# Performance work log

Measured on AMD Instinct MI355X. Metric: run time of the kernel, lower is better.

## Reference

```python
import jax, jax.numpy as jnp
import numpy as np

N_MASTER = 100000
N_BOND = 200000
N_GLOB = 5000
E1 = 400000
E2 = 100000
D_IN = 64
D_OUT = 64
H = 4
SLOPE = 0.2  # leaky relu negative slope


def _mlp(x, W0, b0, W1, b1, W2):
    # LinearN with num_fc_layers=3: ELU, ELU, Identity (last layer no bias)
    h = jax.nn.elu(x @ W0 + b0)
    h = jax.nn.elu(h @ W1 + b1)
    return h @ W2  # (N, H*D_OUT)


def setup_inputs() -> dict:
    key = jax.random.key(0)
    ks = jax.random.split(key, 32)
    s = 0.1  # weight scale
    d = {
        "master_feats": jax.random.normal(ks[0], (N_MASTER, D_IN), jnp.float32),
        "bond_feats": jax.random.normal(ks[1], (N_BOND, D_IN), jnp.float32),
        "global_feats": jax.random.normal(ks[2], (N_GLOB, D_IN), jnp.float32),
        "atom_W0": jax.random.normal(ks[3], (D_IN, D_OUT), jnp.float32) * s,
        "atom_b0": jnp.zeros((D_OUT,), jnp.float32),
        "atom_W1": jax.random.normal(ks[4], (D_OUT, D_OUT), jnp.float32) * s,
        "atom_b1": jnp.zeros((D_OUT,), jnp.float32),
        "atom_W2": jax.random.normal(ks[5], (D_OUT, H * D_OUT), jnp.float32) * s,
        "bond_W0": jax.random.normal(ks[6], (D_IN, D_OUT), jnp.float32) * s,
        "bond_b0": jnp.zeros((D_OUT,), jnp.float32),
        "bond_W1": jax.random.normal(ks[7], (D_OUT, D_OUT), jnp.float32) * s,
        "bond_b1": jnp.zeros((D_OUT,), jnp.float32),
        "bond_W2": jax.random.normal(ks[8], (D_OUT, H * D_OUT), jnp.float32) * s,
        "glob_W0": jax.random.normal(ks[9], (D_IN, D_OUT), jnp.float32) * s,
        "glob_b0": jnp.zeros((D_OUT,), jnp.float32),
        "glob_W1": jax.random.normal(ks[10], (D_OUT, D_OUT), jnp.float32) * s,
        "glob_b1": jnp.zeros((D_OUT,), jnp.float32),
        "glob_W2": jax.random.normal(ks[11], (D_OUT, H * D_OUT), jnp.float32) * s,
        "attn_l": jax.random.normal(ks[12], (H, D_OUT), jnp.float32) * s,
        "attn_r": jax.random.normal(ks[13], (H, D_OUT), jnp.float32) * s,
        "e1_src": jax.random.randint(ks[14], (E1,), 0, N_BOND, jnp.int32),
        "e1_dst": jax.random.randint(ks[15], (E1,), 0, N_MASTER, jnp.int32),
        "e2_src": jax.random.randint(ks[16], (E2,), 0, N_GLOB, jnp.int32),
        "e2_dst": jax.random.randint(ks[17], (E2,), 0, N_MASTER, jnp.int32),
    }
    return d


def reference(master_feats, bond_feats, global_feats,
              atom_W0, atom_b0, atom_W1, atom_b1, atom_W2,
              bond_W0, bond_b0, bond_W1, bond_b1, bond_W2,
              glob_W0, glob_b0, glob_W1, glob_b1, glob_W2,
              attn_l, attn_r, e1_src, e1_dst, e2_src, e2_dst):
    # Per-node-type projections to (N, H, D_OUT)
    ft_m = _mlp(master_feats, atom_W0, atom_b0, atom_W1, atom_b1, atom_W2).reshape(N_MASTER, H, D_OUT)
    ft_b = _mlp(bond_feats, bond_W0, bond_b0, bond_W1, bond_b1, bond_W2).reshape(N_BOND, H, D_OUT)
    ft_g = _mlp(global_feats, glob_W0, glob_b0, glob_W1, glob_b1, glob_W2).reshape(N_GLOB, H, D_OUT)

    er = jnp.einsum('nhd,hd->nh', ft_m, attn_r)  # master (dst) scores
    el_b = jnp.einsum('nhd,hd->nh', ft_b, attn_l)
    el_g = jnp.einsum('nhd,hd->nh', ft_g, attn_l)

    # Per-edge logits: u_add_v then leaky relu
    e1 = jax.nn.leaky_relu(el_b[e1_src] + er[e1_dst], negative_slope=SLOPE)  # (E1, H)
    e2 = jax.nn.leaky_relu(el_g[e2_src] + er[e2_dst], negative_slope=SLOPE)  # (E2, H)

    # Joint edge softmax over all incoming edges per master node
    dst_all = jnp.concatenate([e1_dst, e2_dst])  # (E1+E2,)
    e_all = jnp.concatenate([e1, e2], axis=0)    # (E1+E2, H)
    emax = jax.ops.segment_max(e_all, dst_all, num_segments=N_MASTER)  # (N, H)
    ex = jnp.exp(e_all - emax[dst_all])
    esum = jax.ops.segment_sum(ex, dst_all, num_segments=N_MASTER)     # (N, H)
    a = ex / esum[dst_all]                                             # (E, H)

    # Aggregate: u_mul_e, sum per destination master node
    src_ft = jnp.concatenate([ft_b[e1_src], ft_g[e2_src]], axis=0)     # (E, H, D)
    msgs = src_ft * a[:, :, None]
    rst = jax.ops.segment_sum(msgs, dst_all, num_segments=N_MASTER)    # (N, H, D)
    return rst
```

## Files before the change

kernel.cpp:

```cpp
#include <hip/hip_runtime.h>

#define NM 100000
#define NB 200000
#define NG 5000
#define NE1 400000
#define NE2 100000
#define NE (NE1 + NE2)
#define NMP 100004
#define SCAN_BLOCKS 391

typedef __attribute__((ext_vector_type(8))) short bf16x8;
typedef __attribute__((ext_vector_type(4))) short short4v;
typedef __attribute__((ext_vector_type(4))) float f32x4;

__device__ __forceinline__ unsigned short f2bf(float f) {
    unsigned int u = __float_as_uint(f);
    u += 0x7FFFu + ((u >> 16) & 1u);
    return (unsigned short)(u >> 16);
}
__device__ __forceinline__ float bf2f(unsigned short u) {
    return __uint_as_float((unsigned int)u << 16);
}
__device__ __forceinline__ float elu_f(float x) {
    return x > 0.f ? x : __expf(x) - 1.f;
}
__device__ __forceinline__ char* swz(char* base, int j, int byteoff) {
    return base + j * 128 + ((((byteoff >> 4) ^ (j & 7)) << 4) | (byteoff & 15));
}

struct WEnt { const float* W; short* o; int I; int off; };
struct WAll { WEnt e[9]; };

__global__ __launch_bounds__(256) void wprep_all_kernel(WAll a)
{
    const int idx = blockIdx.x * 256 + threadIdx.x;
    #pragma unroll
    for (int j = 8; j >= 0; --j) {
        if (idx >= a.e[j].off) {
            const int local = idx - a.e[j].off;
            const int I = a.e[j].I;
            const int i = local >> 6, k = local & 63;
            a.e[j].o[local] = (short)f2bf(a.e[j].W[k * I + i]);
            break;
        }
    }
}

__global__ __launch_bounds__(256) void mlp_mfma_kernel(
    const float* __restrict__ x, int N,
    const short* __restrict__ W0t, const float* __restrict__ b0,
    const short* __restrict__ W1t, const float* __restrict__ b1,
    const short* __restrict__ W2t,
    const float* __restrict__ attn,
    float* __restrict__ score,
    unsigned short* __restrict__ ft_out)
{
    __shared__ __attribute__((aligned(128))) char ldsA[64 * 128];
    __shared__ __attribute__((aligned(128))) char ldsB[64 * 128];

    const int tid = threadIdx.x;
    const int w = tid >> 6, l = tid & 63;
    const int g = l >> 4, c = l & 15;
    const int r0 = blockIdx.x << 6;

    {
        const int j = tid >> 2, q = tid & 3;
        const int row = r0 + j;
        bf16x8 o0 = (bf16x8)0, o1 = (bf16x8)0;
        if (row < N) {
            const float4* xp = (const float4*)(x + ((size_t)row << 6) + (q << 4));
            #pragma unroll
            for (int u = 0; u < 2; ++u) {
                float4 v = xp[u];
                o0[u*4+0] = (short)f2bf(v.x); o0[u*4+1] = (short)f2bf(v.y);
                o0[u*4+2] = (short)f2bf(v.z); o0[u*4+3] = (short)f2bf(v.w);
            }
            #pragma unroll
            for (int u = 0; u < 2; ++u) {
                float4 v = xp[u + 2];
                o1[u*4+0] = (short)f2bf(v.x); o1[u*4+1] = (short)f2bf(v.y);
                o1[u*4+2] = (short)f2bf(v.z); o1[u*4+3] = (short)f2bf(v.w);
            }
        }
        *(bf16x8*)swz(ldsA, j, q * 32)      = o0;
        *(bf16x8*)swz(ldsA, j, q * 32 + 16) = o1;
    }
    __syncthreads();

    char* src = ldsA;
    char* dst = ldsB;
    #pragma unroll
    for (int layer = 0; layer < 2; ++layer) {
        const short* Wt = layer ? W1t : W0t;
        const float* bb = layer ? b1 : b0;
        f32x4 acc[4] = {};
        #pragma unroll
        for (int step = 0; step < 2; ++step) {
            bf16x8 a = *(const bf16x8*)(Wt + (((16 * w + c) << 6) + 32 * step + 8 * g));
            #pragma unroll
            for (int t = 0; t < 4; ++t) {
                const int j = 16 * t + c;
                bf16x8 b = *(const bf16x8*)swz(src, j, 64 * step + 16 * g);
                acc[t] = __builtin_amdgcn_mfma_f32_16x16x32_bf16(a, b, acc[t], 0, 0, 0);
            }
        }
        const int i0 = 16 * w + 4 * g;
        const float4 bias = *(const float4*)(bb + i0);
        #pragma unroll
        for (int t = 0; t < 4; ++t) {
            const int j = 16 * t + c;
            short4v o;
            o[0] = (short)f2bf(elu_f(acc[t][0] + bias.x));
            o[1] = (short)f2bf(elu_f(acc[t][1] + bias.y));
            o[2] = (short)f2bf(elu_f(acc[t][2] + bias.z));
            o[3] = (short)f2bf(elu_f(acc[t][3] + bias.w));
            *(short4v*)swz(dst, j, 32 * w + 8 * g) = o;
        }
        __syncthreads();
        char* tmp = src; src = dst; dst = tmp;
    }

    {
        f32x4 acc[4][4] = {};
        #pragma unroll
        for (int step = 0; step < 2; ++step) {
            bf16x8 bfr[4];
            #pragma unroll
            for (int t = 0; t < 4; ++t)
                bfr[t] = *(const bf16x8*)swz(src, 16 * t + c, 64 * step + 16 * g);
            #pragma unroll
            for (int it = 0; it < 4; ++it) {
                bf16x8 a = *(const bf16x8*)(W2t + (((64 * w + 16 * it + c) << 6) + 32 * step + 8 * g));
                #pragma unroll
                for (int t = 0; t < 4; ++t)
                    acc[it][t] = __builtin_amdgcn_mfma_f32_16x16x32_bf16(a, bfr[t], acc[it][t], 0, 0, 0);
            }
        }
        float4 av[4];
        #pragma unroll
        for (int it = 0; it < 4; ++it)
            av[it] = *(const float4*)(attn + 64 * w + 16 * it + 4 * g);

        #pragma unroll
        for (int t = 0; t < 4; ++t) {
            const int row = r0 + 16 * t + c;
            float p = 0.f;
            #pragma unroll
            for (int it = 0; it < 4; ++it) {
                p += acc[it][t][0] * av[it].x + acc[it][t][1] * av[it].y
                   + acc[it][t][2] * av[it].z + acc[it][t][3] * av[it].w;
            }
            p += __shfl_xor(p, 16);
            p += __shfl_xor(p, 32);
            if (row < N) {
                if (g == 0) score[(row << 2) + w] = p;
                if (ft_out) {
                    #pragma unroll
                    for (int it = 0; it < 4; ++it) {
                        short4v o;
                        o[0] = (short)f2bf(acc[it][t][0]);
                        o[1] = (short)f2bf(acc[it][t][1]);
                        o[2] = (short)f2bf(acc[it][t][2]);
                        o[3] = (short)f2bf(acc[it][t][3]);
                        *(short4v*)(ft_out + ((size_t)row << 8) + 64 * w + 16 * it + 4 * g) = o;
                    }
                }
            }
        }
    }
}

__global__ void hist_kernel(const int* __restrict__ e1_dst,
                            const int* __restrict__ e2_dst,
                            int* __restrict__ counts)
{
    int i = blockIdx.x * blockDim.x + threadIdx.x;
    if (i < NE1) atomicAdd(&counts[e1_dst[i]], 1);
    else if (i < NE) atomicAdd(&counts[e2_dst[i - NE1]], 1);
}

__global__ __launch_bounds__(256) void scan1_kernel(
    const int* __restrict__ counts,
    int* __restrict__ prefix_inc,
    int* __restrict__ blocksums)
{
    const int i = blockIdx.x * 256 + threadIdx.x;
    const int lane = threadIdx.x & 63, wv = threadIdx.x >> 6;
    int v = (i < NM) ? counts[i] : 0;
    int x = v;
    #pragma unroll
    for (int o = 1; o < 64; o <<= 1) {
        int u = __shfl_up(x, o);
        if (lane >= o) x += u;
    }
    __shared__ int wsum[4];
    if (lane == 63) wsum[wv] = x;
    __syncthreads();
    int add = 0;
    #pragma unroll
    for (int k = 0; k < 3; ++k) add += (k < wv) ? wsum[k] : 0;
    x += add;
    if (i < NM) prefix_inc[i] = x;
    if (threadIdx.x == 255) blocksums[blockIdx.x] = x;
}

__global__ __launch_bounds__(512) void scan2_kernel(int* __restrict__ blocksums)
{
    const int t = threadIdx.x;
    const int lane = t & 63, wv = t >> 6;
    int v = (t < SCAN_BLOCKS) ? blocksums[t] : 0;
    int x = v;
    #pragma unroll
    for (int o = 1; o < 64; o <<= 1) {
        int u = __shfl_up(x, o);
        if (lane >= o) x += u;
    }
    __shared__ int wsum[8];
    if (lane == 63) wsum[wv] = x;
    __syncthreads();
    int add = 0;
    #pragma unroll
    for (int k = 0; k < 7; ++k) add += (k < wv) ? wsum[k] : 0;
    x += add;
    if (t < SCAN_BLOCKS) blocksums[t] = x - v;
}

__global__ __launch_bounds__(256) void scan3_kernel(
    const int* __restrict__ counts,
    const int* __restrict__ prefix_inc,
    const int* __restrict__ blocksums,
    int* __restrict__ offsets,
    int* __restrict__ cursor)
{
    const int i = blockIdx.x * 256 + threadIdx.x;
    if (i > NM) return;
    if (i == NM) { offsets[NM] = NE; return; }
    const int off = prefix_inc[i] - counts[i] + blocksums[blockIdx.x];
    offsets[i] = off;
    cursor[i]  = off;
}

__global__ void fill_kernel(const int* __restrict__ e1_src,
                            const int* __restrict__ e1_dst,
                            const int* __restrict__ e2_src,
                            const int* __restrict__ e2_dst,
                            const float* __restrict__ er,
                            const float* __restrict__ el_b,
                            const float* __restrict__ el_g,
                            int* __restrict__ cursor,
                            int* __restrict__ sorted,
                            float4* __restrict__ vsort)
{
    int i = blockIdx.x * blockDim.x + threadIdx.x;
    if (i >= NE) return;
    int dst, src, enc;
    const float* el;
    if (i < NE1) { src = e1_src[i]; dst = e1_dst[i]; enc = src;              el = el_b; }
    else { int j = i - NE1; src = e2_src[j]; dst = e2_dst[j]; enc = src | (1 << 30); el = el_g; }
    const float4 l4 = *(const float4*)(el + (src << 2));
    const float4 r4 = *(const float4*)(er + (dst << 2));
    float4 v;
    v.x = l4.x + r4.x; v.x = v.x > 0.f ? v.x : 0.2f * v.x;
    v.y = l4.y + r4.y; v.y = v.y > 0.f ? v.y : 0.2f * v.y;
    v.z = l4.z + r4.z; v.z = v.z > 0.f ? v.z : 0.2f * v.z;
    v.w = l4.w + r4.w; v.w = v.w > 0.f ? v.w : 0.2f * v.w;
    int p = atomicAdd(&cursor[dst], 1);
    sorted[p] = enc;
    vsort[p] = v;
}

__global__ __launch_bounds__(256) void aggregate_kernel(
    const int* __restrict__ offsets,
    const int* __restrict__ sorted,
    const float* __restrict__ vsort,
    const unsigned short* __restrict__ ftb,
    const unsigned short* __restrict__ ftg,
    float* __restrict__ out)
{
    const int w = threadIdx.x >> 6, l = threadIdx.x & 63;
    const int h  = l >> 4;
    const int f4 = l << 2;

    const int n = (blockIdx.x << 2) + w;
    if (n >= NM) return;

    const int start = offsets[n];
    const int deg   = offsets[n + 1] - start;

    float ax = 0.f, ay = 0.f, az = 0.f, aw = 0.f;
    if (deg > 0) {
        float m = -1e30f;
        for (int e = 0; e < deg; ++e)
            m = fmaxf(m, vsort[((start + e) << 2) + h]);

        float s = 0.f;
        for (int e = 0; e < deg; ++e) {
            const float wgt = __expf(vsort[((start + e) << 2) + h] - m);
            s += wgt;
            const int enc = sorted[start + e];
            const int isg = enc >> 30;
            const int src = enc & 0x3FFFFFFF;
            const unsigned short* ft =
                (isg ? ftg : ftb) + ((size_t)src << 8) + f4;
            const short4v u = *(const short4v*)ft;
            ax = fmaf(bf2f((unsigned short)u[0]), wgt, ax);
            ay = fmaf(bf2f((unsigned short)u[1]), wgt, ay);
            az = fmaf(bf2f((unsigned short)u[2]), wgt, az);
            aw = fmaf(bf2f((unsigned short)u[3]), wgt, aw);
        }
        const float inv = 1.f / s;
        ax *= inv; ay *= inv; az *= inv; aw *= inv;
    }
    float4 o = make_float4(ax, ay, az, aw);
    *(float4*)(out + ((size_t)n << 8) + f4) = o;
}

extern "C" void kernel_launch(void* const* d_in, const int* in_sizes, int n_in,
                              void* d_out, int out_size, void* d_ws, size_t ws_size,
                              hipStream_t stream)
{
    const float* master = (const float*)d_in[0];
    const float* bond   = (const float*)d_in[1];
    const float* glob   = (const float*)d_in[2];
    const float* aW0 = (const float*)d_in[3];
    const float* ab0 = (const float*)d_in[4];
    const float* aW1 = (const float*)d_in[5];
    const float* ab1 = (const float*)d_in[6];
    const float* aW2 = (const float*)d_in[7];
    const float* bW0 = (const float*)d_in[8];
    const float* bb0 = (const float*)d_in[9];
    const float* bW1 = (const float*)d_in[10];
    const float* bb1 = (const float*)d_in[11];
    const float* bW2 = (const float*)d_in[12];
    const float* gW0 = (const float*)d_in[13];
    const float* gb0 = (const float*)d_in[14];
    const float* gW1 = (const float*)d_in[15];
    const float* gb1 = (const float*)d_in[16];
    const float* gW2 = (const float*)d_in[17];
    const float* attn_l = (const float*)d_in[18];
    const float* attn_r = (const float*)d_in[19];
    const int* e1_src = (const int*)d_in[20];
    const int* e1_dst = (const int*)d_in[21];
    const int* e2_src = (const int*)d_in[22];
    const int* e2_dst = (const int*)d_in[23];
    float* out = (float*)d_out;

    float* ws   = (float*)d_ws;
    unsigned short* ft_b = (unsigned short*)ws;
    unsigned short* ft_g = ft_b + (size_t)NB * 256;
    float* er   = (float*)(ft_g + (size_t)NG * 256);
    float* el_b = er + (size_t)NM * 4;
    float* el_g = el_b + (size_t)NB * 4;
    int* counts  = (int*)(el_g + (size_t)NG * 4);
    int* offsets = counts + NMP;
    int* cursor  = offsets + NMP;
    int* sorted  = cursor + NMP;
    float4* vsort = (float4*)(sorted + NE);
    int* prefix_inc = (int*)(vsort + NE);
    int* blocksums  = prefix_inc + NMP;
    short* wtA = (short*)(blocksums + 512);
    short* wtB = wtA + 24576;
    short* wtG = wtB + 24576;

    hipMemsetAsync(counts, 0, sizeof(int) * NM, stream);

    WAll wa;
    wa.e[0] = {aW0, wtA,          64,     0};
    wa.e[1] = {aW1, wtA + 4096,   64,  4096};
    wa.e[2] = {aW2, wtA + 8192,  256,  8192};
    wa.e[3] = {bW0, wtB,          64, 24576};
    wa.e[4] = {bW1, wtB + 4096,   64, 28672};
    wa.e[5] = {bW2, wtB + 8192,  256, 32768};
    wa.e[6] = {gW0, wtG,          64, 49152};
    wa.e[7] = {gW1, wtG + 4096,   64, 53248};
    wa.e[8] = {gW2, wtG + 8192,  256, 57344};
    wprep_all_kernel<<<288, 256, 0, stream>>>(wa);

    mlp_mfma_kernel<<<(NM + 63) / 64, 256, 0, stream>>>(
        master, NM, wtA, ab0, wtA + 4096, ab1, wtA + 8192, attn_r, er, nullptr);
    mlp_mfma_kernel<<<(NB + 63) / 64, 256, 0, stream>>>(
        bond, NB, wtB, bb0, wtB + 4096, bb1, wtB + 8192, attn_l, el_b, ft_b);
    mlp_mfma_kernel<<<(NG + 63) / 64, 256, 0, stream>>>(
        glob, NG, wtG, gb0, wtG + 4096, gb1, wtG + 8192, attn_l, el_g, ft_g);

    hist_kernel<<<(NE + 255) / 256, 256, 0, stream>>>(e1_dst, e2_dst, counts);
    scan1_kernel<<<SCAN_BLOCKS, 256, 0, stream>>>(counts, prefix_inc, blocksums);
    scan2_kernel<<<1, 512, 0, stream>>>(blocksums);
    scan3_kernel<<<SCAN_BLOCKS + 1, 256, 0, stream>>>(counts, prefix_inc, blocksums,
                                                      offsets, cursor);
    fill_kernel<<<(NE + 255) / 256, 256, 0, stream>>>(e1_src, e1_dst, e2_src, e2_dst,
                                                      er, el_b, el_g,
                                                      cursor, sorted, vsort);
    aggregate_kernel<<<(NM + 3) / 4, 256, 0, stream>>>(offsets, sorted,
                                                       (const float*)vsort,
                                                       ft_b, ft_g, out);
}
```

Baseline: 250.4 us.

## Precompute per-node max via atomics and software-pipeline aggregate gathers

The per-destination softmax max is now computed in fill_kernel with four order-preserving-key atomicMax operations per edge, so aggregate no longer needs a separate pass over each node's edges to find the max. The aggregate loop is software-pipelined: the edge index and logit are prefetched two edges ahead and the feature row one edge ahead, hiding gather latency behind the accumulate. Feature and output writes become nontemporal stores. The cost is 2M extra atomics in fill, plus a larger memset and workspace for the max keys.

```diff
diff --git a/kernel.cpp b/kernel.cpp
--- a/kernel.cpp
+++ b/kernel.cpp
@@ -23,6 +23,14 @@
 }
 __device__ __forceinline__ float elu_f(float x) {
     return x > 0.f ? x : __expf(x) - 1.f;
+}
+__device__ __forceinline__ unsigned int fkey(float f) {
+    unsigned int u = __float_as_uint(f);
+    return (u & 0x80000000u) ? ~u : (u | 0x80000000u);
+}
+__device__ __forceinline__ float keydec(unsigned int k) {
+    unsigned int u = (k & 0x80000000u) ? (k & 0x7FFFFFFFu) : ~k;
+    return __uint_as_float(u);
 }
 __device__ __forceinline__ char* swz(char* base, int j, int byteoff) {
     return base + j * 128 + ((((byteoff >> 4) ^ (j & 7)) << 4) | (byteoff & 15));
@@ -162,7 +170,8 @@
                         o[1] = (short)f2bf(acc[it][t][1]);
                         o[2] = (short)f2bf(acc[it][t][2]);
                         o[3] = (short)f2bf(acc[it][t][3]);
-                        *(short4v*)(ft_out + ((size_t)row << 8) + 64 * w + 16 * it + 4 * g) = o;
+                        __builtin_nontemporal_store(o,
+                            (short4v*)(ft_out + ((size_t)row << 8) + 64 * w + 16 * it + 4 * g));
                     }
                 }
             }
@@ -249,7 +258,8 @@
                             const float* __restrict__ el_g,
                             int* __restrict__ cursor,
                             int* __restrict__ sorted,
-                            float4* __restrict__ vsort)
+                            float4* __restrict__ vsort,
+                            unsigned int* __restrict__ maxkey)
 {
     int i = blockIdx.x * blockDim.x + threadIdx.x;
     if (i >= NE) return;
@@ -264,6 +274,11 @@
     v.y = l4.y + r4.y; v.y = v.y > 0.f ? v.y : 0.2f * v.y;
     v.z = l4.z + r4.z; v.z = v.z > 0.f ? v.z : 0.2f * v.z;
     v.w = l4.w + r4.w; v.w = v.w > 0.f ? v.w : 0.2f * v.w;
+    unsigned int* mk = maxkey + ((size_t)dst << 2);
+    atomicMax(&mk[0], fkey(v.x));
+    atomicMax(&mk[1], fkey(v.y));
+    atomicMax(&mk[2], fkey(v.z));
+    atomicMax(&mk[3], fkey(v.w));
     int p = atomicAdd(&cursor[dst], 1);
     sorted[p] = enc;
     vsort[p] = v;
@@ -273,6 +288,7 @@
     const int* __restrict__ offsets,
     const int* __restrict__ sorted,
     const float* __restrict__ vsort,
+    const unsigned int* __restrict__ maxkey,
     const unsigned short* __restrict__ ftb,
     const unsigned short* __restrict__ ftg,
     float* __restrict__ out)
@@ -287,32 +303,41 @@
     const int start = offsets[n];
     const int deg   = offsets[n + 1] - start;
 
-    float ax = 0.f, ay = 0.f, az = 0.f, aw = 0.f;
+    f32x4 o = {};
     if (deg > 0) {
-        float m = -1e30f;
-        for (int e = 0; e < deg; ++e)
-            m = fmaxf(m, vsort[((start + e) << 2) + h]);
+        const float m = keydec(maxkey[((size_t)n << 2) + h]);
+
+        int   encA = sorted[start];
+        float vA   = vsort[(start << 2) + h];
+        const int i1 = start + (deg > 1 ? 1 : 0);
+        int   encB = sorted[i1];
+        float vB   = vsort[(i1 << 2) + h];
+        const unsigned short* pA =
+            ((encA >> 30) ? ftg : ftb) + (((size_t)(encA & 0x3FFFFFFF)) << 8) + f4;
+        short4v ftA = *(const short4v*)pA;
 
         float s = 0.f;
         for (int e = 0; e < deg; ++e) {
-            const float wgt = __expf(vsort[((start + e) << 2) + h] - m);
+            const int i2 = start + min(e + 2, deg - 1);
+            const int   encC = sorted[i2];
+            const float vC   = vsort[(i2 << 2) + h];
+            const unsigned short* pB =
+                ((encB >> 30) ? ftg : ftb) + (((size_t)(encB & 0x3FFFFFFF)) << 8) + f4;
+            const short4v ftB = *(const short4v*)pB;
+
+            const float wgt = __expf(vA - m);
             s += wgt;
-            const int enc = sorted[start + e];
-            const int isg = enc >> 30;
-            const int src = enc & 0x3FFFFFFF;
-            const unsigned short* ft =
-                (isg ? ftg : ftb) + ((size_t)src << 8) + f4;
-            const short4v u = *(const short4v*)ft;
-            ax = fmaf(bf2f((unsigned short)u[0]), wgt, ax);
-            ay = fmaf(bf2f((unsigned short)u[1]), wgt, ay);
-            az = fmaf(bf2f((unsigned short)u[2]), wgt, az);
-            aw = fmaf(bf2f((unsigned short)u[3]), wgt, aw);
+            o[0] = fmaf(bf2f((unsigned short)ftA[0]), wgt, o[0]);
+            o[1] = fmaf(bf2f((unsigned short)ftA[1]), wgt, o[1]);
+            o[2] = fmaf(bf2f((unsigned short)ftA[2]), wgt, o[2]);
+            o[3] = fmaf(bf2f((unsigned short)ftA[3]), wgt, o[3]);
+
+            ftA = ftB; vA = vB; encB = encC; vB = vC;
         }
         const float inv = 1.f / s;
-        ax *= inv; ay *= inv; az *= inv; aw *= inv;
-    }
-    float4 o = make_float4(ax, ay, az, aw);
-    *(float4*)(out + ((size_t)n << 8) + f4) = o;
+        o[0] *= inv; o[1] *= inv; o[2] *= inv; o[3] *= inv;
+    }
+    __builtin_nontemporal_store(o, (f32x4*)(out + ((size_t)n << 8) + f4));
 }
 
 extern "C" void kernel_launch(void* const* d_in, const int* in_sizes, int n_in,
@@ -352,7 +377,8 @@
     float* el_b = er + (size_t)NM * 4;
     float* el_g = el_b + (size_t)NB * 4;
     int* counts  = (int*)(el_g + (size_t)NG * 4);
-    int* offsets = counts + NMP;
+    unsigned int* maxkey = (unsigned int*)(counts + NMP);
+    int* offsets = (int*)(maxkey + (size_t)NM * 4);
     int* cursor  = offsets + NMP;
     int* sorted  = cursor + NMP;
     float4* vsort = (float4*)(sorted + NE);
@@ -362,7 +388,7 @@
     short* wtB = wtA + 24576;
     short* wtG = wtB + 24576;
 
-    hipMemsetAsync(counts, 0, sizeof(int) * NM, stream);
+    hipMemsetAsync(counts, 0, sizeof(int) * (NMP + (size_t)NM * 4), stream);
 
     WAll wa;
     wa.e[0] = {aW0, wtA,          64,     0};
@@ -390,8 +416,8 @@
                                                       offsets, cursor);
     fill_kernel<<<(NE + 255) / 256, 256, 0, stream>>>(e1_src, e1_dst, e2_src, e2_dst,
                                                       er, el_b, el_g,
-                                                      cursor, sorted, vsort);
+                                                      cursor, sorted, vsort, maxkey);
     aggregate_kernel<<<(NM + 3) / 4, 256, 0, stream>>>(offsets, sorted,
-                                                       (const float*)vsort,
+                                                       (const float*)vsort, maxkey,
                                                        ft_b, ft_g, out);
 }
```

Measured after the change: 312.9 us. 25.0% more time.
